# Optimization experiments

Hardware: AMD Instinct MI355X
Metric: run time of the kernel (lower is better)

## Reference

```python
import jax, jax.numpy as jnp
import numpy as np

N, D = 2048, 64


def setup_inputs() -> dict:
    key = jax.random.key(0)
    x = jax.random.normal(key, (N, D), dtype=jnp.float32)
    return {"x": x}


def reference(x):
    # torch scan over rows i: rd_i = sqrt(sum((x - x_i)^2, axis=1))
    # Stacked result is the full self-cdist matrix [N, N].
    diff = x[:, None, :] - x[None, :, :]        # [N, N, D] (row i = samex - x_i)
    sq_sum = jnp.sum(diff * diff, axis=-1)      # [N, N]
    return jnp.sqrt(sq_sum)
```

## Files before the change

kernel.cpp:

```cpp
#include <hip/hip_runtime.h>
#include <math.h>

#define NN 2048
#define DD 64
#define BT 64
#define LDK 72

typedef short short8 __attribute__((ext_vector_type(8)));
typedef float f32x4 __attribute__((ext_vector_type(4)));
typedef unsigned short us4 __attribute__((ext_vector_type(4)));

__device__ inline unsigned short f2bf(float f) {
    unsigned u = __float_as_uint(f);
    return (unsigned short)((u + 0x7FFFu + ((u >> 16) & 1u)) >> 16);
}

__global__ __launch_bounds__(256, 6) void cdist_bf16(const float* __restrict__ x,
                                                     float* __restrict__ out) {
    __shared__ unsigned short CA[BT][LDK];
    __shared__ unsigned short CB[BT][LDK];
    __shared__ float nrmA[BT], nrmB[BT];

    const int tid = threadIdx.x;
    const int bi = blockIdx.y * BT;
    const int bj = blockIdx.x * BT;

    #pragma unroll
    for (int p = 0; p < 2; ++p) {
        const float4* src = (const float4*)(x + (size_t)(p ? bj : bi) * DD);
        unsigned short (*C)[LDK] = p ? CB : CA;
        float* nr = p ? nrmB : nrmA;
        #pragma unroll
        for (int s = 0; s < 4; ++s) {
            int idx = tid + s * 256;
            int row = idx >> 4;
            int c4  = (idx & 15) << 2;
            float4 v = src[idx];
            us4 hv = {f2bf(v.x), f2bf(v.y), f2bf(v.z), f2bf(v.w)};
            *(us4*)(&C[row][c4]) = hv;
            float sum = v.x * v.x;
            sum = fmaf(v.y, v.y, sum);
            sum = fmaf(v.z, v.z, sum);
            sum = fmaf(v.w, v.w, sum);
            sum += __shfl_xor(sum, 1, 16);
            sum += __shfl_xor(sum, 2, 16);
            sum += __shfl_xor(sum, 4, 16);
            sum += __shfl_xor(sum, 8, 16);
            if ((tid & 15) == 0) nr[row] = sum;
        }
    }
    __syncthreads();

    const int lane = tid & 63;
    const int wid  = tid >> 6;
    const int wm = wid >> 1, wn = wid & 1;
    const int lr = lane & 15;
    const int lk = (lane >> 4) * 8;

    f32x4 acc[2][2] = {};
    #pragma unroll
    for (int ks = 0; ks < 2; ++ks) {
        const int k = ks * 32 + lk;
        short8 a0 = *(const short8*)(&CA[wm * 32 + lr][k]);
        short8 a1 = *(const short8*)(&CA[wm * 32 + 16 + lr][k]);
        short8 b0 = *(const short8*)(&CB[wn * 32 + lr][k]);
        short8 b1 = *(const short8*)(&CB[wn * 32 + 16 + lr][k]);
        acc[0][0] = __builtin_amdgcn_mfma_f32_16x16x32_bf16(a0, b0, acc[0][0], 0, 0, 0);
        acc[0][1] = __builtin_amdgcn_mfma_f32_16x16x32_bf16(a0, b1, acc[0][1], 0, 0, 0);
        acc[1][0] = __builtin_amdgcn_mfma_f32_16x16x32_bf16(a1, b0, acc[1][0], 0, 0, 0);
        acc[1][1] = __builtin_amdgcn_mfma_f32_16x16x32_bf16(a1, b1, acc[1][1], 0, 0, 0);
    }

    const float nb0 = nrmB[wn * 32 + lr];
    const float nb1 = nrmB[wn * 32 + 16 + lr];
    #pragma unroll
    for (int m = 0; m < 2; ++m) {
        #pragma unroll
        for (int g = 0; g < 4; ++g) {
            const int row = wm * 32 + m * 16 + (lane >> 4) * 4 + g;
            const int gi  = bi + row;
            const float na = nrmA[row];
            float* orow = out + (size_t)gi * NN + bj;
            const int col0 = wn * 32 + lr;
            const int col1 = col0 + 16;
            float v0 = na + nb0 - 2.f * acc[m][0][g];
            float v1 = na + nb1 - 2.f * acc[m][1][g];
            orow[col0] = (gi == bj + col0) ? 0.f : sqrtf(fmaxf(v0, 0.f));
            orow[col1] = (gi == bj + col1) ? 0.f : sqrtf(fmaxf(v1, 0.f));
        }
    }
}

extern "C" void kernel_launch(void* const* d_in, const int* in_sizes, int n_in,
                              void* d_out, int out_size, void* d_ws, size_t ws_size,
                              hipStream_t stream) {
    const float* x = (const float*)d_in[0];
    float* out = (float*)d_out;
    dim3 grid(NN / BT, NN / BT);
    cdist_bf16<<<grid, dim3(256), 0, stream>>>(x, out);
}
```

Measured before the change: 13.46 us.

## Exploit distance-matrix symmetry: compute upper-triangle tiles and mirror stores

```diff
diff --git a/kernel.cpp b/kernel.cpp
--- a/kernel.cpp
+++ b/kernel.cpp
@@ -4,6 +4,7 @@
 #define NN 2048
 #define DD 64
 #define BT 64
+#define NB (NN / BT)
 #define LDK 72
 
 typedef short short8 __attribute__((ext_vector_type(8)));
@@ -15,15 +16,19 @@
     return (unsigned short)((u + 0x7FFFu + ((u >> 16) & 1u)) >> 16);
 }
 
-__global__ __launch_bounds__(256, 6) void cdist_bf16(const float* __restrict__ x,
-                                                     float* __restrict__ out) {
+__global__ __launch_bounds__(256, 6) void cdist_sym(const float* __restrict__ x,
+                                                    float* __restrict__ out) {
     __shared__ unsigned short CA[BT][LDK];
     __shared__ unsigned short CB[BT][LDK];
     __shared__ float nrmA[BT], nrmB[BT];
 
+    int u = 0, rem = blockIdx.x, cnt = NB;
+    while (rem >= cnt) { rem -= cnt; ++u; --cnt; }
+    const int v = u + rem;
+    const int bi = u * BT;
+    const int bj = v * BT;
+
     const int tid = threadIdx.x;
-    const int bi = blockIdx.y * BT;
-    const int bj = blockIdx.x * BT;
 
     #pragma unroll
     for (int p = 0; p < 2; ++p) {
@@ -35,13 +40,13 @@
             int idx = tid + s * 256;
             int row = idx >> 4;
             int c4  = (idx & 15) << 2;
-            float4 v = src[idx];
-            us4 hv = {f2bf(v.x), f2bf(v.y), f2bf(v.z), f2bf(v.w)};
+            float4 vv = src[idx];
+            us4 hv = {f2bf(vv.x), f2bf(vv.y), f2bf(vv.z), f2bf(vv.w)};
             *(us4*)(&C[row][c4]) = hv;
-            float sum = v.x * v.x;
-            sum = fmaf(v.y, v.y, sum);
-            sum = fmaf(v.z, v.z, sum);
-            sum = fmaf(v.w, v.w, sum);
+            float sum = vv.x * vv.x;
+            sum = fmaf(vv.y, vv.y, sum);
+            sum = fmaf(vv.z, vv.z, sum);
+            sum = fmaf(vv.w, vv.w, sum);
             sum += __shfl_xor(sum, 1, 16);
             sum += __shfl_xor(sum, 2, 16);
             sum += __shfl_xor(sum, 4, 16);
@@ -71,22 +76,27 @@
         acc[1][1] = __builtin_amdgcn_mfma_f32_16x16x32_bf16(a1, b1, acc[1][1], 0, 0, 0);
     }
 
-    const float nb0 = nrmB[wn * 32 + lr];
-    const float nb1 = nrmB[wn * 32 + 16 + lr];
+    const float nb[2] = { nrmB[wn * 32 + lr], nrmB[wn * 32 + 16 + lr] };
+    const int rbase = wm * 32 + (lane >> 4) * 4;
     #pragma unroll
     for (int m = 0; m < 2; ++m) {
         #pragma unroll
-        for (int g = 0; g < 4; ++g) {
-            const int row = wm * 32 + m * 16 + (lane >> 4) * 4 + g;
-            const int gi  = bi + row;
-            const float na = nrmA[row];
-            float* orow = out + (size_t)gi * NN + bj;
-            const int col0 = wn * 32 + lr;
-            const int col1 = col0 + 16;
-            float v0 = na + nb0 - 2.f * acc[m][0][g];
-            float v1 = na + nb1 - 2.f * acc[m][1][g];
-            orow[col0] = (gi == bj + col0) ? 0.f : sqrtf(fmaxf(v0, 0.f));
-            orow[col1] = (gi == bj + col1) ? 0.f : sqrtf(fmaxf(v1, 0.f));
+        for (int n = 0; n < 2; ++n) {
+            const int col = wn * 32 + n * 16 + lr;
+            const int gj  = bj + col;
+            f32x4 fd;
+            #pragma unroll
+            for (int g = 0; g < 4; ++g) {
+                const int row = rbase + m * 16 + g;
+                const int gi  = bi + row;
+                float vv = nrmA[row] + nb[n] - 2.f * acc[m][n][g];
+                float d = sqrtf(fmaxf(vv, 0.f));
+                d = (gi == gj) ? 0.f : d;
+                fd[g] = d;
+                __builtin_nontemporal_store(d, out + (size_t)gi * NN + gj);
+            }
+            __builtin_nontemporal_store(
+                fd, (f32x4*)(out + (size_t)gj * NN + bi + rbase + m * 16));
         }
     }
 }
@@ -96,6 +106,5 @@
                               hipStream_t stream) {
     const float* x = (const float*)d_in[0];
     float* out = (float*)d_out;
-    dim3 grid(NN / BT, NN / BT);
-    cdist_bf16<<<grid, dim3(256), 0, stream>>>(x, out);
+    cdist_sym<<<dim3(NB * (NB + 1) / 2), dim3(256), 0, stream>>>(x, out);
 }
```

New measurement: 12.28 us (median of 2 runs). -8.8%, faster.
